# Performance work log

Hardware: AMD Instinct MI355X
Metric: run time of the kernel (lower is better)

## Reference

```python
import jax, jax.numpy as jnp
import numpy as np

EPS = 1e-6

def setup_inputs() -> dict:
    key = jax.random.key(0)
    ks = jax.random.split(key, 4)
    T, B, D, N = 512, 16, 1024, 512
    # xavier-uniform-ish scale for projections
    lim = float(np.sqrt(6.0 / (N + D)))
    x = jax.random.normal(ks[0], (T, B, D), dtype=jnp.float32)
    W_k = jax.random.uniform(ks[1], (N, D), minval=-lim, maxval=lim, dtype=jnp.float32)
    W_v = jax.random.uniform(ks[2], (N, D), minval=-lim, maxval=lim, dtype=jnp.float32)
    W_q = jax.random.uniform(ks[3], (N, D), minval=-lim, maxval=lim, dtype=jnp.float32)
    return {"x": x, "W_k": W_k, "W_v": W_v, "W_q": W_q}

def reference(x, W_k, W_v, W_q):
    # x: (T, B, D); delta-rule fast-weight cell, proj=no_z, nonlin=tanh,
    # gate=output, update=delta.
    T, B, D = x.shape
    n = W_k.shape[0]
    k = jnp.einsum('tbd,nd->tbn', x, W_k)
    v = jnp.einsum('tbd,nd->tbn', x, W_v)
    q = jnp.einsum('tbd,nd->tbn', x, W_q)
    k_norm = k / (jnp.linalg.norm(k, axis=-1, keepdims=True) + EPS)

    def step(S, kvq):
        k_t, v_t, q_t = kvq  # each (B, n)
        retrieved = jnp.einsum('bij,bj->bi', S, k_t)
        delta = v_t - retrieved
        S_new = jnp.tanh(S + delta[:, :, None] * k_t[:, None, :])
        Sq = jnp.einsum('bij,bj->bi', S_new, q_t)
        out = Sq * jax.nn.silu(Sq)
        return S_new, out

    S0 = jnp.zeros((B, n, n), dtype=x.dtype)
    S_final, outputs = jax.lax.scan(step, S0, (k_norm, v, q))
    return outputs, S_final
```

## Files before the change

### kernel.cpp

```cpp
#include <hip/hip_runtime.h>
#include <hip/hip_bf16.h>

#define T_DIM 512
#define B_DIM 16
#define D_DIM 1024
#define N_DIM 512

#define C_FOLD  2.885390082f
#define INV_C   0.3465735903f

typedef short s16x8 __attribute__((ext_vector_type(8)));
typedef float f32x4 __attribute__((ext_vector_type(4)));
typedef float f32x2 __attribute__((ext_vector_type(2)));

__device__ __forceinline__ unsigned short f2bf(float f) {
    unsigned u = __float_as_uint(f);
    unsigned r = (u + 0x7fffu + ((u >> 16) & 1u)) >> 16;
    return (unsigned short)r;
}

__device__ __forceinline__ float half32_sum(float x) {
    x += __int_as_float(__builtin_amdgcn_update_dpp(0, __float_as_int(x), 0xB1,  0xf, 0xf, true));
    x += __int_as_float(__builtin_amdgcn_update_dpp(0, __float_as_int(x), 0x4E,  0xf, 0xf, true));
    x += __int_as_float(__builtin_amdgcn_update_dpp(0, __float_as_int(x), 0x124, 0xf, 0xf, true));
    x += __int_as_float(__builtin_amdgcn_update_dpp(0, __float_as_int(x), 0x128, 0xf, 0xf, true));
    x += __int_as_float(__builtin_amdgcn_ds_swizzle(__float_as_int(x), 0x401F));
    return x;
}

__global__ __launch_bounds__(256) void proj_gemm(
    const float* __restrict__ x,
    const float* __restrict__ Wk,
    const float* __restrict__ Wv,
    const float* __restrict__ Wq,
    float* __restrict__ kbuf, float* __restrict__ vbuf, float* __restrict__ qbuf)
{
    const float* W = (blockIdx.z == 0) ? Wk : (blockIdx.z == 1) ? Wv : Wq;
    float* out = (blockIdx.z == 0) ? kbuf : (blockIdx.z == 1) ? vbuf : qbuf;

    __shared__ __align__(16) unsigned short As[64 * 40];
    __shared__ __align__(16) unsigned short Bs[64 * 40];

    const int tid  = threadIdx.x;
    const int m0   = blockIdx.x * 64;
    const int n0   = blockIdx.y * 64;
    const int wave = tid >> 6;
    const int lane = tid & 63;
    const int l15  = lane & 15;
    const int quad = lane >> 4;

    const int srow = tid >> 2;
    const int scol = (tid & 3) * 8;

    f32x4 acc[4];
#pragma unroll
    for (int i = 0; i < 4; ++i) acc[i] = (f32x4)0.0f;

    for (int k0 = 0; k0 < D_DIM; k0 += 32) {
        __syncthreads();
        {
            const float* srcA = &x[(size_t)(m0 + srow) * D_DIM + k0 + scol];
            float4 a0 = *(const float4*)srcA;
            float4 a1 = *(const float4*)(srcA + 4);
            uint4 pa;
            pa.x = (unsigned)f2bf(a0.x) | ((unsigned)f2bf(a0.y) << 16);
            pa.y = (unsigned)f2bf(a0.z) | ((unsigned)f2bf(a0.w) << 16);
            pa.z = (unsigned)f2bf(a1.x) | ((unsigned)f2bf(a1.y) << 16);
            pa.w = (unsigned)f2bf(a1.z) | ((unsigned)f2bf(a1.w) << 16);
            *(uint4*)&As[srow * 40 + scol] = pa;

            const float* srcB = &W[(size_t)(n0 + srow) * D_DIM + k0 + scol];
            float4 b0 = *(const float4*)srcB;
            float4 b1 = *(const float4*)(srcB + 4);
            uint4 pb;
            pb.x = (unsigned)f2bf(b0.x) | ((unsigned)f2bf(b0.y) << 16);
            pb.y = (unsigned)f2bf(b0.z) | ((unsigned)f2bf(b0.w) << 16);
            pb.z = (unsigned)f2bf(b1.x) | ((unsigned)f2bf(b1.y) << 16);
            pb.w = (unsigned)f2bf(b1.z) | ((unsigned)f2bf(b1.w) << 16);
            *(uint4*)&Bs[srow * 40 + scol] = pb;
        }
        __syncthreads();
        s16x8 af = *(const s16x8*)&As[(wave * 16 + l15) * 40 + quad * 8];
#pragma unroll
        for (int nt = 0; nt < 4; ++nt) {
            s16x8 bf = *(const s16x8*)&Bs[(nt * 16 + l15) * 40 + quad * 8];
            acc[nt] = __builtin_amdgcn_mfma_f32_16x16x32_bf16(af, bf, acc[nt], 0, 0, 0);
        }
    }
#pragma unroll
    for (int nt = 0; nt < 4; ++nt) {
#pragma unroll
        for (int rg = 0; rg < 4; ++rg) {
            int row = m0 + wave * 16 + quad * 4 + rg;
            int col = n0 + nt * 16 + l15;
            out[(size_t)row * N_DIM + col] = acc[nt][rg];
        }
    }
}

__global__ __launch_bounds__(256) void knorm(float* __restrict__ kbuf)
{
    const int wave = threadIdx.x >> 6;
    const int lane = threadIdx.x & 63;
    const int row  = blockIdx.x * 4 + wave;
    float* p = &kbuf[(size_t)row * N_DIM + lane * 8];
    float4 a = *(const float4*)p;
    float4 b = *(const float4*)(p + 4);
    float s = a.x*a.x + a.y*a.y + a.z*a.z + a.w*a.w
            + b.x*b.x + b.y*b.y + b.z*b.z + b.w*b.w;
#pragma unroll
    for (int m = 1; m < 64; m <<= 1) s += __shfl_xor(s, m, 64);
    float inv = 1.0f / (sqrtf(s) + 1e-6f);
    a.x *= inv; a.y *= inv; a.z *= inv; a.w *= inv;
    b.x *= inv; b.y *= inv; b.z *= inv; b.w *= inv;
    *(float4*)p = a;
    *(float4*)(p + 4) = b;
}

__global__ __launch_bounds__(256) void scan_kernel(
    const float* __restrict__ kbuf, const float* __restrict__ vbuf,
    const float* __restrict__ qbuf, float* __restrict__ out)
{
    __shared__ __align__(16) float ks[2][576];
    __shared__ __align__(16) float qs[2][576];
    __shared__ float vs[2][16];

    const int tid  = threadIdx.x;
    const int lane = tid & 63;
    const int wv   = tid >> 6;
    const int h    = lane >> 5;
    const int tj   = lane & 31;
    const int b    = blockIdx.y;
    const int i0   = blockIdx.x * 16;
    const int r0   = 4 * wv + 2 * h;

    const int wA = 36 * (tid >> 4) + ((2 * tid) & 31);
    const int rA = 36 * (tj >> 1) + 16 * (tj & 1);

    f32x2 SA[8], SB[8];
#pragma unroll
    for (int u = 0; u < 8; ++u) { SA[u] = (f32x2)0.0f; SB[u] = (f32x2)0.0f; }

    float2 pk, pq; float pv = 0.0f;
    {
        const size_t o0 = (size_t)b * N_DIM;
        pk = *(const float2*)&kbuf[o0 + 2 * tid];
        pq = *(const float2*)&qbuf[o0 + 2 * tid];
        if (tid < 16) pv = vbuf[o0 + i0 + tid];
        *(float2*)&ks[0][wA] = pk;
        *(float2*)&qs[0][wA] = pq;
        if (tid < 16) vs[0][tid] = pv;
        const size_t o1 = (size_t)(B_DIM + b) * N_DIM;
        pk = *(const float2*)&kbuf[o1 + 2 * tid];
        pq = *(const float2*)&qbuf[o1 + 2 * tid];
        if (tid < 16) pv = vbuf[o1 + i0 + tid];
    }
    __syncthreads();

    const f32x2 Cv   = {C_FOLD, C_FOLD};
    const f32x2 M2Cv = {-2.0f * C_FOLD, -2.0f * C_FOLD};

    for (int t = 0; t < T_DIM; ++t) {
        const int cb = t & 1, nb = cb ^ 1;
        const size_t ofs = ((size_t)t * B_DIM + b) * N_DIM;

        if (t + 1 < T_DIM) {
            *(float2*)&ks[nb][wA] = pk;
            *(float2*)&qs[nb][wA] = pq;
            if (tid < 16) vs[nb][tid] = pv;
        }
        if (t + 2 < T_DIM) {
            const size_t o2 = ((size_t)(t + 2) * B_DIM + b) * N_DIM;
            pk = *(const float2*)&kbuf[o2 + 2 * tid];
            pq = *(const float2*)&qbuf[o2 + 2 * tid];
            if (tid < 16) pv = vbuf[o2 + i0 + tid];
        }

        f32x2 k2[8], q2[8];
#pragma unroll
        for (int u = 0; u < 4; ++u) {
            f32x4 kv = *(const f32x4*)&ks[cb][rA + 4 * u];
            f32x4 qv = *(const f32x4*)&qs[cb][rA + 4 * u];
            k2[2*u] = kv.xy; k2[2*u+1] = kv.zw;
            q2[2*u] = qv.xy; q2[2*u+1] = qv.zw;
        }
        const float v0 = vs[cb][r0];
        const float v1 = vs[cb][r0 + 1];

        f32x2 pa0 = (f32x2)0.0f, pb0 = (f32x2)0.0f;
        f32x2 pa1 = (f32x2)0.0f, pb1 = (f32x2)0.0f;
#pragma unroll
        for (int u = 0; u < 8; u += 2) {
            pa0 += SA[u] * k2[u];  pb0 += SA[u + 1] * k2[u + 1];
            pa1 += SB[u] * k2[u];  pb1 += SB[u + 1] * k2[u + 1];
        }
        const float racc0 = half32_sum(pa0.x + pa0.y + pb0.x + pb0.y);
        const float racc1 = half32_sum(pa1.x + pa1.y + pb1.x + pb1.y);

        const float dp0 = __builtin_fmaf(C_FOLD, v0, -racc0);
        const float dp1 = __builtin_fmaf(C_FOLD, v1, -racc1);
        const f32x2 d0 = {dp0, dp0}, d1 = {dp1, dp1};

        f32x2 sa0 = (f32x2)0.0f, sb0 = (f32x2)0.0f;
        f32x2 sa1 = (f32x2)0.0f, sb1 = (f32x2)0.0f;
#pragma unroll
        for (int u = 0; u < 8; u += 2) {
            f32x2 aA0 = SA[u]     + d0 * k2[u];
            f32x2 aB0 = SB[u]     + d1 * k2[u];
            f32x2 aA1 = SA[u + 1] + d0 * k2[u + 1];
            f32x2 aB1 = SB[u + 1] + d1 * k2[u + 1];
            f32x2 eA0 = { __builtin_amdgcn_exp2f(aA0.x), __builtin_amdgcn_exp2f(aA0.y) };
            f32x2 eB0 = { __builtin_amdgcn_exp2f(aB0.x), __builtin_amdgcn_exp2f(aB0.y) };
            f32x2 eA1 = { __builtin_amdgcn_exp2f(aA1.x), __builtin_amdgcn_exp2f(aA1.y) };
            f32x2 eB1 = { __builtin_amdgcn_exp2f(aB1.x), __builtin_amdgcn_exp2f(aB1.y) };
            eA0 = eA0 + 1.0f; eB0 = eB0 + 1.0f; eA1 = eA1 + 1.0f; eB1 = eB1 + 1.0f;
            f32x2 rA0 = { __builtin_amdgcn_rcpf(eA0.x), __builtin_amdgcn_rcpf(eA0.y) };
            f32x2 rB0 = { __builtin_amdgcn_rcpf(eB0.x), __builtin_amdgcn_rcpf(eB0.y) };
            f32x2 rA1 = { __builtin_amdgcn_rcpf(eA1.x), __builtin_amdgcn_rcpf(eA1.y) };
            f32x2 rB1 = { __builtin_amdgcn_rcpf(eB1.x), __builtin_amdgcn_rcpf(eB1.y) };
            f32x2 nA0 = Cv + rA0 * M2Cv;
            f32x2 nB0 = Cv + rB0 * M2Cv;
            f32x2 nA1 = Cv + rA1 * M2Cv;
            f32x2 nB1 = Cv + rB1 * M2Cv;
            SA[u] = nA0; SB[u] = nB0; SA[u + 1] = nA1; SB[u + 1] = nB1;
            sa0 += nA0 * q2[u];     sa1 += nB0 * q2[u];
            sb0 += nA1 * q2[u + 1]; sb1 += nB1 * q2[u + 1];
        }
        const float sq0 = half32_sum(sa0.x + sa0.y + sb0.x + sb0.y);
        const float sq1 = half32_sum(sa1.x + sa1.y + sb1.x + sb1.y);

        if (tj == 0) {
            float s0 = sq0 * INV_C, s1 = sq1 * INV_C;
            float g0 = __builtin_amdgcn_rcpf(1.0f + __builtin_amdgcn_exp2f(-s0 * 1.44269504f));
            float g1 = __builtin_amdgcn_rcpf(1.0f + __builtin_amdgcn_exp2f(-s1 * 1.44269504f));
            out[ofs + i0 + r0]     = s0 * s0 * g0;
            out[ofs + i0 + r0 + 1] = s1 * s1 * g1;
        }
        __syncthreads();
    }

    const size_t base = (size_t)T_DIM * B_DIM * N_DIM;
    const size_t so0 = base + ((size_t)b * N_DIM + i0 + r0) * N_DIM + 16 * tj;
    const size_t so1 = so0 + N_DIM;
#pragma unroll
    for (int u = 0; u < 4; ++u) {
        float4 w0, w1;
        w0.x = SA[2*u].x   * INV_C; w0.y = SA[2*u].y   * INV_C;
        w0.z = SA[2*u+1].x * INV_C; w0.w = SA[2*u+1].y * INV_C;
        w1.x = SB[2*u].x   * INV_C; w1.y = SB[2*u].y   * INV_C;
        w1.z = SB[2*u+1].x * INV_C; w1.w = SB[2*u+1].y * INV_C;
        *(float4*)&out[so0 + 4 * u] = w0;
        *(float4*)&out[so1 + 4 * u] = w1;
    }
}

extern "C" void kernel_launch(void* const* d_in, const int* in_sizes, int n_in,
                              void* d_out, int out_size, void* d_ws, size_t ws_size,
                              hipStream_t stream) {
    const float* x  = (const float*)d_in[0];
    const float* Wk = (const float*)d_in[1];
    const float* Wv = (const float*)d_in[2];
    const float* Wq = (const float*)d_in[3];
    float* outp = (float*)d_out;

    const size_t MN = (size_t)T_DIM * B_DIM * N_DIM;
    float* kbuf = (float*)d_ws;
    float* vbuf = kbuf + MN;
    float* qbuf = vbuf + MN;

    proj_gemm<<<dim3(128, 8, 3), 256, 0, stream>>>(x, Wk, Wv, Wq, kbuf, vbuf, qbuf);
    knorm<<<2048, 256, 0, stream>>>(kbuf);
    scan_kernel<<<dim3(32, 16), 256, 0, stream>>>(kbuf, vbuf, qbuf, outp);
}
```

Measured before the change: 785.8 us.

## Halve rows per scan block to double grid and shorten per-step critical path

Result: slower. 807.1 us (+2.7%).

```diff
diff --git a/kernel.cpp b/kernel.cpp
--- a/kernel.cpp
+++ b/kernel.cpp
@@ -123,37 +123,35 @@
 {
     __shared__ __align__(16) float ks[2][576];
     __shared__ __align__(16) float qs[2][576];
-    __shared__ float vs[2][16];
+    __shared__ float vs[2][8];
 
     const int tid  = threadIdx.x;
     const int lane = tid & 63;
-    const int wv   = tid >> 6;
-    const int h    = lane >> 5;
     const int tj   = lane & 31;
     const int b    = blockIdx.y;
-    const int i0   = blockIdx.x * 16;
-    const int r0   = 4 * wv + 2 * h;
+    const int i0   = blockIdx.x * 8;
+    const int r0   = tid >> 5;
 
     const int wA = 36 * (tid >> 4) + ((2 * tid) & 31);
     const int rA = 36 * (tj >> 1) + 16 * (tj & 1);
 
-    f32x2 SA[8], SB[8];
-#pragma unroll
-    for (int u = 0; u < 8; ++u) { SA[u] = (f32x2)0.0f; SB[u] = (f32x2)0.0f; }
+    f32x2 SA[8];
+#pragma unroll
+    for (int u = 0; u < 8; ++u) SA[u] = (f32x2)0.0f;
 
     float2 pk, pq; float pv = 0.0f;
     {
         const size_t o0 = (size_t)b * N_DIM;
         pk = *(const float2*)&kbuf[o0 + 2 * tid];
         pq = *(const float2*)&qbuf[o0 + 2 * tid];
-        if (tid < 16) pv = vbuf[o0 + i0 + tid];
+        if (tid < 8) pv = vbuf[o0 + i0 + tid];
         *(float2*)&ks[0][wA] = pk;
         *(float2*)&qs[0][wA] = pq;
-        if (tid < 16) vs[0][tid] = pv;
+        if (tid < 8) vs[0][tid] = pv;
         const size_t o1 = (size_t)(B_DIM + b) * N_DIM;
         pk = *(const float2*)&kbuf[o1 + 2 * tid];
         pq = *(const float2*)&qbuf[o1 + 2 * tid];
-        if (tid < 16) pv = vbuf[o1 + i0 + tid];
+        if (tid < 8) pv = vbuf[o1 + i0 + tid];
     }
     __syncthreads();
 
@@ -167,13 +165,13 @@
         if (t + 1 < T_DIM) {
             *(float2*)&ks[nb][wA] = pk;
             *(float2*)&qs[nb][wA] = pq;
-            if (tid < 16) vs[nb][tid] = pv;
+            if (tid < 8) vs[nb][tid] = pv;
         }
         if (t + 2 < T_DIM) {
             const size_t o2 = ((size_t)(t + 2) * B_DIM + b) * N_DIM;
             pk = *(const float2*)&kbuf[o2 + 2 * tid];
             pq = *(const float2*)&qbuf[o2 + 2 * tid];
-            if (tid < 16) pv = vbuf[o2 + i0 + tid];
+            if (tid < 8) pv = vbuf[o2 + i0 + tid];
         }
 
         f32x2 k2[8], q2[8];
@@ -185,72 +183,52 @@
             q2[2*u] = qv.xy; q2[2*u+1] = qv.zw;
         }
         const float v0 = vs[cb][r0];
-        const float v1 = vs[cb][r0 + 1];
-
-        f32x2 pa0 = (f32x2)0.0f, pb0 = (f32x2)0.0f;
-        f32x2 pa1 = (f32x2)0.0f, pb1 = (f32x2)0.0f;
+
+        f32x2 pa = (f32x2)0.0f, pb = (f32x2)0.0f;
 #pragma unroll
         for (int u = 0; u < 8; u += 2) {
-            pa0 += SA[u] * k2[u];  pb0 += SA[u + 1] * k2[u + 1];
-            pa1 += SB[u] * k2[u];  pb1 += SB[u + 1] * k2[u + 1];
-        }
-        const float racc0 = half32_sum(pa0.x + pa0.y + pb0.x + pb0.y);
-        const float racc1 = half32_sum(pa1.x + pa1.y + pb1.x + pb1.y);
-
-        const float dp0 = __builtin_fmaf(C_FOLD, v0, -racc0);
-        const float dp1 = __builtin_fmaf(C_FOLD, v1, -racc1);
-        const f32x2 d0 = {dp0, dp0}, d1 = {dp1, dp1};
-
-        f32x2 sa0 = (f32x2)0.0f, sb0 = (f32x2)0.0f;
-        f32x2 sa1 = (f32x2)0.0f, sb1 = (f32x2)0.0f;
+            pa += SA[u]     * k2[u];
+            pb += SA[u + 1] * k2[u + 1];
+        }
+        const float racc = half32_sum(pa.x + pa.y + pb.x + pb.y);
+
+        const float dp = __builtin_fmaf(C_FOLD, v0, -racc);
+        const f32x2 d0 = {dp, dp};
+
+        f32x2 sa = (f32x2)0.0f, sb = (f32x2)0.0f;
 #pragma unroll
         for (int u = 0; u < 8; u += 2) {
-            f32x2 aA0 = SA[u]     + d0 * k2[u];
-            f32x2 aB0 = SB[u]     + d1 * k2[u];
-            f32x2 aA1 = SA[u + 1] + d0 * k2[u + 1];
-            f32x2 aB1 = SB[u + 1] + d1 * k2[u + 1];
-            f32x2 eA0 = { __builtin_amdgcn_exp2f(aA0.x), __builtin_amdgcn_exp2f(aA0.y) };
-            f32x2 eB0 = { __builtin_amdgcn_exp2f(aB0.x), __builtin_amdgcn_exp2f(aB0.y) };
-            f32x2 eA1 = { __builtin_amdgcn_exp2f(aA1.x), __builtin_amdgcn_exp2f(aA1.y) };
-            f32x2 eB1 = { __builtin_amdgcn_exp2f(aB1.x), __builtin_amdgcn_exp2f(aB1.y) };
-            eA0 = eA0 + 1.0f; eB0 = eB0 + 1.0f; eA1 = eA1 + 1.0f; eB1 = eB1 + 1.0f;
-            f32x2 rA0 = { __builtin_amdgcn_rcpf(eA0.x), __builtin_amdgcn_rcpf(eA0.y) };
-            f32x2 rB0 = { __builtin_amdgcn_rcpf(eB0.x), __builtin_amdgcn_rcpf(eB0.y) };
-            f32x2 rA1 = { __builtin_amdgcn_rcpf(eA1.x), __builtin_amdgcn_rcpf(eA1.y) };
-            f32x2 rB1 = { __builtin_amdgcn_rcpf(eB1.x), __builtin_amdgcn_rcpf(eB1.y) };
-            f32x2 nA0 = Cv + rA0 * M2Cv;
-            f32x2 nB0 = Cv + rB0 * M2Cv;
-            f32x2 nA1 = Cv + rA1 * M2Cv;
-            f32x2 nB1 = Cv + rB1 * M2Cv;
-            SA[u] = nA0; SB[u] = nB0; SA[u + 1] = nA1; SB[u + 1] = nB1;
-            sa0 += nA0 * q2[u];     sa1 += nB0 * q2[u];
-            sb0 += nA1 * q2[u + 1]; sb1 += nB1 * q2[u + 1];
-        }
-        const float sq0 = half32_sum(sa0.x + sa0.y + sb0.x + sb0.y);
-        const float sq1 = half32_sum(sa1.x + sa1.y + sb1.x + sb1.y);
+            f32x2 a0 = SA[u]     + d0 * k2[u];
+            f32x2 a1 = SA[u + 1] + d0 * k2[u + 1];
+            f32x2 e0 = { __builtin_amdgcn_exp2f(a0.x), __builtin_amdgcn_exp2f(a0.y) };
+            f32x2 e1 = { __builtin_amdgcn_exp2f(a1.x), __builtin_amdgcn_exp2f(a1.y) };
+            e0 = e0 + 1.0f; e1 = e1 + 1.0f;
+            f32x2 rc0 = { __builtin_amdgcn_rcpf(e0.x), __builtin_amdgcn_rcpf(e0.y) };
+            f32x2 rc1 = { __builtin_amdgcn_rcpf(e1.x), __builtin_amdgcn_rcpf(e1.y) };
+            f32x2 n0 = Cv + rc0 * M2Cv;
+            f32x2 n1 = Cv + rc1 * M2Cv;
+            SA[u] = n0; SA[u + 1] = n1;
+            sa += n0 * q2[u];
+            sb += n1 * q2[u + 1];
+        }
+        const float sq = half32_sum(sa.x + sa.y + sb.x + sb.y);
 
         if (tj == 0) {
-            float s0 = sq0 * INV_C, s1 = sq1 * INV_C;
+            float s0 = sq * INV_C;
             float g0 = __builtin_amdgcn_rcpf(1.0f + __builtin_amdgcn_exp2f(-s0 * 1.44269504f));
-            float g1 = __builtin_amdgcn_rcpf(1.0f + __builtin_amdgcn_exp2f(-s1 * 1.44269504f));
-            out[ofs + i0 + r0]     = s0 * s0 * g0;
-            out[ofs + i0 + r0 + 1] = s1 * s1 * g1;
+            out[ofs + i0 + r0] = s0 * s0 * g0;
         }
         __syncthreads();
     }
 
     const size_t base = (size_t)T_DIM * B_DIM * N_DIM;
     const size_t so0 = base + ((size_t)b * N_DIM + i0 + r0) * N_DIM + 16 * tj;
-    const size_t so1 = so0 + N_DIM;
 #pragma unroll
     for (int u = 0; u < 4; ++u) {
-        float4 w0, w1;
+        float4 w0;
         w0.x = SA[2*u].x   * INV_C; w0.y = SA[2*u].y   * INV_C;
         w0.z = SA[2*u+1].x * INV_C; w0.w = SA[2*u+1].y * INV_C;
-        w1.x = SB[2*u].x   * INV_C; w1.y = SB[2*u].y   * INV_C;
-        w1.z = SB[2*u+1].x * INV_C; w1.w = SB[2*u+1].y * INV_C;
         *(float4*)&out[so0 + 4 * u] = w0;
-        *(float4*)&out[so1 + 4 * u] = w1;
     }
 }
 
@@ -270,5 +248,5 @@
 
     proj_gemm<<<dim3(128, 8, 3), 256, 0, stream>>>(x, Wk, Wv, Wq, kbuf, vbuf, qbuf);
     knorm<<<2048, 256, 0, stream>>>(kbuf);
-    scan_kernel<<<dim3(32, 16), 256, 0, stream>>>(kbuf, vbuf, qbuf, outp);
-}
+    scan_kernel<<<dim3(64, 16), 256, 0, stream>>>(kbuf, vbuf, qbuf, outp);
+}
```

## Give each wave private LDS copies of k/q and drop per-step block barrier

Applied to the files above, without the earlier changes.

After: 800.4 us. No clear change (+1.9%).

```diff
diff --git a/kernel.cpp b/kernel.cpp
--- a/kernel.cpp
+++ b/kernel.cpp
@@ -121,9 +121,8 @@
     const float* __restrict__ kbuf, const float* __restrict__ vbuf,
     const float* __restrict__ qbuf, float* __restrict__ out)
 {
-    __shared__ __align__(16) float ks[2][576];
-    __shared__ __align__(16) float qs[2][576];
-    __shared__ float vs[2][16];
+    __shared__ __align__(16) float ks[4][2][576];
+    __shared__ __align__(16) float qs[4][2][576];
 
     const int tid  = threadIdx.x;
     const int lane = tid & 63;
@@ -134,28 +133,35 @@
     const int i0   = blockIdx.x * 16;
     const int r0   = 4 * wv + 2 * h;
 
-    const int wA = 36 * (tid >> 4) + ((2 * tid) & 31);
+    const int wA = 36 * (lane >> 2) + ((8 * lane) & 31);
     const int rA = 36 * (tj >> 1) + 16 * (tj & 1);
 
     f32x2 SA[8], SB[8];
 #pragma unroll
     for (int u = 0; u < 8; ++u) { SA[u] = (f32x2)0.0f; SB[u] = (f32x2)0.0f; }
 
-    float2 pk, pq; float pv = 0.0f;
+    float4 pka, pkb, pqa, pqb;
+    float va0, va1, vb0, vb1;
     {
-        const size_t o0 = (size_t)b * N_DIM;
-        pk = *(const float2*)&kbuf[o0 + 2 * tid];
-        pq = *(const float2*)&qbuf[o0 + 2 * tid];
-        if (tid < 16) pv = vbuf[o0 + i0 + tid];
-        *(float2*)&ks[0][wA] = pk;
-        *(float2*)&qs[0][wA] = pq;
-        if (tid < 16) vs[0][tid] = pv;
-        const size_t o1 = (size_t)(B_DIM + b) * N_DIM;
-        pk = *(const float2*)&kbuf[o1 + 2 * tid];
-        pq = *(const float2*)&qbuf[o1 + 2 * tid];
-        if (tid < 16) pv = vbuf[o1 + i0 + tid];
-    }
-    __syncthreads();
+        const size_t o0 = (size_t)b * N_DIM + 8 * lane;
+        pka = *(const float4*)&kbuf[o0];
+        pkb = *(const float4*)&kbuf[o0 + 4];
+        pqa = *(const float4*)&qbuf[o0];
+        pqb = *(const float4*)&qbuf[o0 + 4];
+        *(float4*)&ks[wv][0][wA]     = pka;
+        *(float4*)&ks[wv][0][wA + 4] = pkb;
+        *(float4*)&qs[wv][0][wA]     = pqa;
+        *(float4*)&qs[wv][0][wA + 4] = pqb;
+        const size_t o1 = ((size_t)B_DIM + b) * N_DIM + 8 * lane;
+        pka = *(const float4*)&kbuf[o1];
+        pkb = *(const float4*)&kbuf[o1 + 4];
+        pqa = *(const float4*)&qbuf[o1];
+        pqb = *(const float4*)&qbuf[o1 + 4];
+        const size_t v0o = (size_t)b * N_DIM + i0 + r0;
+        const size_t v1o = ((size_t)B_DIM + b) * N_DIM + i0 + r0;
+        va0 = vbuf[v0o]; va1 = vbuf[v0o + 1];
+        vb0 = vbuf[v1o]; vb1 = vbuf[v1o + 1];
+    }
 
     const f32x2 Cv   = {C_FOLD, C_FOLD};
     const f32x2 M2Cv = {-2.0f * C_FOLD, -2.0f * C_FOLD};
@@ -165,27 +171,32 @@
         const size_t ofs = ((size_t)t * B_DIM + b) * N_DIM;
 
         if (t + 1 < T_DIM) {
-            *(float2*)&ks[nb][wA] = pk;
-            *(float2*)&qs[nb][wA] = pq;
-            if (tid < 16) vs[nb][tid] = pv;
-        }
+            *(float4*)&ks[wv][nb][wA]     = pka;
+            *(float4*)&ks[wv][nb][wA + 4] = pkb;
+            *(float4*)&qs[wv][nb][wA]     = pqa;
+            *(float4*)&qs[wv][nb][wA + 4] = pqb;
+        }
+        float vt0 = 0.0f, vt1 = 0.0f;
         if (t + 2 < T_DIM) {
             const size_t o2 = ((size_t)(t + 2) * B_DIM + b) * N_DIM;
-            pk = *(const float2*)&kbuf[o2 + 2 * tid];
-            pq = *(const float2*)&qbuf[o2 + 2 * tid];
-            if (tid < 16) pv = vbuf[o2 + i0 + tid];
+            pka = *(const float4*)&kbuf[o2 + 8 * lane];
+            pkb = *(const float4*)&kbuf[o2 + 8 * lane + 4];
+            pqa = *(const float4*)&qbuf[o2 + 8 * lane];
+            pqb = *(const float4*)&qbuf[o2 + 8 * lane + 4];
+            vt0 = vbuf[o2 + i0 + r0];
+            vt1 = vbuf[o2 + i0 + r0 + 1];
         }
 
         f32x2 k2[8], q2[8];
 #pragma unroll
         for (int u = 0; u < 4; ++u) {
-            f32x4 kv = *(const f32x4*)&ks[cb][rA + 4 * u];
-            f32x4 qv = *(const f32x4*)&qs[cb][rA + 4 * u];
+            f32x4 kv = *(const f32x4*)&ks[wv][cb][rA + 4 * u];
+            f32x4 qv = *(const f32x4*)&qs[wv][cb][rA + 4 * u];
             k2[2*u] = kv.xy; k2[2*u+1] = kv.zw;
             q2[2*u] = qv.xy; q2[2*u+1] = qv.zw;
         }
-        const float v0 = vs[cb][r0];
-        const float v1 = vs[cb][r0 + 1];
+        const float v0 = va0;
+        const float v1 = va1;
 
         f32x2 pa0 = (f32x2)0.0f, pb0 = (f32x2)0.0f;
         f32x2 pa1 = (f32x2)0.0f, pb1 = (f32x2)0.0f;
@@ -236,7 +247,8 @@
             out[ofs + i0 + r0]     = s0 * s0 * g0;
             out[ofs + i0 + r0 + 1] = s1 * s1 * g1;
         }
-        __syncthreads();
+
+        va0 = vb0; va1 = vb1; vb0 = vt0; vb1 = vt1;
     }
 
     const size_t base = (size_t)T_DIM * B_DIM * N_DIM;
```
